# Kernel optimization log

Hardware: AMD Instinct MI355X
Metric: run time of the kernel (lower is better)

The kernel has to match this reference:

```python
import jax, jax.numpy as jnp
import numpy as np

NUM_DAYOFWEEK, NUM_TIME, NUM_MONTH, NUM_DAY = 7, 24, 12, 31
NUM_DESTINATION = 100000
NUM_FACTOR = 128
NUM_DIM = NUM_FACTOR // 4  # 32
N = 1048576


def setup_inputs() -> dict:
    key = jax.random.key(0)
    ks = jax.random.split(key, 10)
    std = 0.1
    return {
        "dayofweek": jax.random.randint(ks[0], (N,), 0, NUM_DAYOFWEEK),
        "time": jax.random.randint(ks[1], (N,), 0, NUM_TIME),
        "month": jax.random.randint(ks[2], (N,), 0, NUM_MONTH),
        "day": jax.random.randint(ks[3], (N,), 0, NUM_DAY),
        "destination": jax.random.randint(ks[4], (N,), 0, NUM_DESTINATION),
        "W_dayofweek": std * jax.random.normal(ks[5], (NUM_DAYOFWEEK, NUM_DIM), dtype=jnp.float32),
        "W_time": std * jax.random.normal(ks[6], (NUM_TIME, NUM_DIM), dtype=jnp.float32),
        "W_month": std * jax.random.normal(ks[7], (NUM_MONTH, NUM_DIM), dtype=jnp.float32),
        "W_day": std * jax.random.normal(ks[8], (NUM_DAY, NUM_DIM), dtype=jnp.float32),
        "W_item": std * jax.random.normal(ks[9], (NUM_DESTINATION, NUM_FACTOR), dtype=jnp.float32),
    }


def reference(dayofweek, time, month, day, destination,
              W_dayofweek, W_time, W_month, W_day, W_item) -> jnp.ndarray:
    # Gather per-feature embeddings and concat into user vector [N, num_factor]
    user = jnp.concatenate([
        W_dayofweek[dayofweek],  # [N, 32]
        W_time[time],            # [N, 32]
        W_month[month],          # [N, 32]
        W_day[day],              # [N, 32]
    ], axis=-1)
    item = W_item[destination]   # [N, 128]
    # Original: diagonal(mm(user, item.T)) == rowwise dot product; compute it directly.
    return jnp.sum(user * item, axis=-1)  # [N]
```

## Files before the change

### kernel.cpp

```cpp
#include <hip/hip_runtime.h>


constexpr int NDIM = 32;
constexpr int SZ_DOW = 7 * NDIM;
constexpr int SZ_TIM = 24 * NDIM;
constexpr int SZ_MON = 12 * NDIM;
constexpr int SZ_DAY = 31 * NDIM;
constexpr int B_DOW = 0;
constexpr int B_TIM = B_DOW + SZ_DOW;
constexpr int B_MON = B_TIM + SZ_TIM;
constexpr int B_DAY = B_MON + SZ_MON;
constexpr int TAB_TOT = B_DAY + SZ_DAY;

__global__ __launch_bounds__(256)
void pack_kernel(const int* __restrict__ dow, const int* __restrict__ tim,
                 const int* __restrict__ mon, const int* __restrict__ day,
                 int* __restrict__ packed, int n) {
    int i = blockIdx.x * blockDim.x + threadIdx.x;
    int stride = gridDim.x * blockDim.x;
    for (; i < n; i += stride)
        packed[i] = dow[i] | (tim[i] << 8) | (mon[i] << 16) | (day[i] << 24);
}

__global__ __launch_bounds__(256, 4)
void mf_mlp_kernel(const int* __restrict__ packed, const int* __restrict__ dest,
                   const float* __restrict__ Wdow, const float* __restrict__ Wtim,
                   const float* __restrict__ Wmon, const float* __restrict__ Wday,
                   const float* __restrict__ Witem,
                   float* __restrict__ out, int n)
{
    __shared__ float tab[TAB_TOT];
    const int tid = threadIdx.x;
    for (int i = tid; i < SZ_DOW; i += 256) tab[B_DOW + i] = Wdow[i];
    for (int i = tid; i < SZ_TIM; i += 256) tab[B_TIM + i] = Wtim[i];
    for (int i = tid; i < SZ_MON; i += 256) tab[B_MON + i] = Wmon[i];
    for (int i = tid; i < SZ_DAY; i += 256) tab[B_DAY + i] = Wday[i];
    __syncthreads();

    const int sub = tid & 63;
    const int wv  = tid >> 6;
    const int g   = sub >> 3;
    const int col = (sub & 7) * 4;
    const int l8  = sub & 7;
    const int tb[4] = {B_DOW, B_TIM, B_MON, B_DAY};

    const long gw     = (long)blockIdx.x * 4 + wv;
    const long nwaves = (long)gridDim.x * 4;

    for (long base = gw * 16; base < n; base += nwaves * 16) {
        const long n0 = base + g;
        const long n1 = base + 8 + g;
        const bool v0 = n0 < n, v1 = n1 < n;

        const int pk0 = v0 ? packed[n0] : 0;
        const int d0  = v0 ? dest[n0]   : 0;
        const int pk1 = v1 ? packed[n1] : 0;
        const int d1  = v1 ? dest[n1]   : 0;

        const float* r0 = Witem + (long)d0 * 128 + col;
        const float* r1 = Witem + (long)d1 * 128 + col;

        float4 it0[4], it1[4], us0[4], us1[4];
#pragma unroll
        for (int j = 0; j < 4; j++) it0[j] = *reinterpret_cast<const float4*>(r0 + j * NDIM);
#pragma unroll
        for (int j = 0; j < 4; j++) it1[j] = *reinterpret_cast<const float4*>(r1 + j * NDIM);
#pragma unroll
        for (int j = 0; j < 4; j++) {
            const int idx = (pk0 >> (8 * j)) & 0xFF;
            us0[j] = *reinterpret_cast<const float4*>(&tab[tb[j] + idx * NDIM + col]);
        }
#pragma unroll
        for (int j = 0; j < 4; j++) {
            const int idx = (pk1 >> (8 * j)) & 0xFF;
            us1[j] = *reinterpret_cast<const float4*>(&tab[tb[j] + idx * NDIM + col]);
        }

        float p0 = 0.f, p1 = 0.f;
#pragma unroll
        for (int j = 0; j < 4; j++) {
            p0 += it0[j].x * us0[j].x + it0[j].y * us0[j].y
                + it0[j].z * us0[j].z + it0[j].w * us0[j].w;
            p1 += it1[j].x * us1[j].x + it1[j].y * us1[j].y
                + it1[j].z * us1[j].z + it1[j].w * us1[j].w;
        }

        p0 += __shfl_xor(p0, 1);  p1 += __shfl_xor(p1, 1);
        p0 += __shfl_xor(p0, 2);  p1 += __shfl_xor(p1, 2);
        p0 += __shfl_xor(p0, 4);  p1 += __shfl_xor(p1, 4);

        if (l8 == 0) {
            if (v0) out[n0] = p0;
            if (v1) out[n1] = p1;
        }
    }
}

__global__ __launch_bounds__(256, 8)
void mf_dot_kernel(const int* __restrict__ dow, const int* __restrict__ tim,
                   const int* __restrict__ mon, const int* __restrict__ day,
                   const int* __restrict__ dest,
                   const float* __restrict__ Wdow, const float* __restrict__ Wtim,
                   const float* __restrict__ Wmon, const float* __restrict__ Wday,
                   const float* __restrict__ Witem,
                   float* __restrict__ out, int n_samples)
{
    __shared__ float tab[TAB_TOT];
    const int tid = threadIdx.x;
    for (int i = tid; i < SZ_DOW; i += 256) tab[B_DOW + i] = Wdow[i];
    for (int i = tid; i < SZ_TIM; i += 256) tab[B_TIM + i] = Wtim[i];
    for (int i = tid; i < SZ_MON; i += 256) tab[B_MON + i] = Wmon[i];
    for (int i = tid; i < SZ_DAY; i += 256) tab[B_DAY + i] = Wday[i];
    __syncthreads();
    const int lane = tid & 63;
    const int sub  = lane & 31;
    const int wave = tid >> 6;
    const int half = lane >> 5;
    const int t    = sub >> 3;
    const int dofs = (sub & 7) * 4;
    const int* idxp  = (t == 0) ? dow   : (t == 1) ? tim   : (t == 2) ? mon   : day;
    const int  tbase = (t == 0) ? B_DOW : (t == 1) ? B_TIM : (t == 2) ? B_MON : B_DAY;
    long n = (long)blockIdx.x * 8 + wave * 2 + half;
    const long stride = (long)gridDim.x * 8;
    for (; n < n_samples; n += stride) {
        const int idx = idxp[n];
        const int ds  = dest[n];
        const float4 u  = *reinterpret_cast<const float4*>(&tab[tbase + idx * NDIM + dofs]);
        const float4 it = *reinterpret_cast<const float4*>(&Witem[(long)ds * 128 + sub * 4]);
        float r = u.x * it.x + u.y * it.y + u.z * it.z + u.w * it.w;
        r += __shfl_xor(r, 16);
        r += __shfl_xor(r, 8);
        r += __shfl_xor(r, 4);
        r += __shfl_xor(r, 2);
        r += __shfl_xor(r, 1);
        if (sub == 0) out[n] = r;
    }
}

extern "C" void kernel_launch(void* const* d_in, const int* in_sizes, int n_in,
                              void* d_out, int out_size, void* d_ws, size_t ws_size,
                              hipStream_t stream)
{
    const int*   dow   = (const int*)d_in[0];
    const int*   tim   = (const int*)d_in[1];
    const int*   mon   = (const int*)d_in[2];
    const int*   day   = (const int*)d_in[3];
    const int*   dest  = (const int*)d_in[4];
    const float* Wdow  = (const float*)d_in[5];
    const float* Wtim  = (const float*)d_in[6];
    const float* Wmon  = (const float*)d_in[7];
    const float* Wday  = (const float*)d_in[8];
    const float* Witem = (const float*)d_in[9];
    float* out = (float*)d_out;

    const int n = in_sizes[0];

    if (ws_size < (size_t)n * sizeof(int)) {
        hipLaunchKernelGGL(mf_dot_kernel, dim3(2048), dim3(256), 0, stream,
                           dow, tim, mon, day, dest,
                           Wdow, Wtim, Wmon, Wday, Witem, out, n);
        return;
    }

    int* packed = (int*)d_ws;
    hipLaunchKernelGGL(pack_kernel, dim3(1024), dim3(256), 0, stream,
                       dow, tim, mon, day, packed, n);
    hipLaunchKernelGGL(mf_mlp_kernel, dim3(2048), dim3(256), 0, stream,
                       packed, dest, Wdow, Wtim, Wmon, Wday, Witem, out, n);
}
```

Measured before the change: 173.8 us.

## Bin samples by destination range for cache-local item table gathers

Replaces the pack+compute pipeline with a counting sort that bins samples into 32 destination ranges (count, scan, scatter of a packed 64-bit payload holding sample index, destination and feature indices). The compute kernel then assigns each block a slice of one bin, with blocks mapped across bins, so concurrent item-row gathers hit a narrow range of W_item that may stay in L2/MALL. The cost is three extra launches, a single-block serial scan, atomics in the scatter, an 8-byte payload written and read per sample, and scattered output writes.

```diff
diff --git a/kernel.cpp b/kernel.cpp
--- a/kernel.cpp
+++ b/kernel.cpp
@@ -2,32 +2,90 @@
 
 
 constexpr int NDIM = 32;
-constexpr int SZ_DOW = 7 * NDIM;
-constexpr int SZ_TIM = 24 * NDIM;
-constexpr int SZ_MON = 12 * NDIM;
-constexpr int SZ_DAY = 31 * NDIM;
+constexpr int SZ_DOW = 7 * NDIM, SZ_TIM = 24 * NDIM, SZ_MON = 12 * NDIM, SZ_DAY = 31 * NDIM;
 constexpr int B_DOW = 0;
 constexpr int B_TIM = B_DOW + SZ_DOW;
 constexpr int B_MON = B_TIM + SZ_TIM;
 constexpr int B_DAY = B_MON + SZ_MON;
 constexpr int TAB_TOT = B_DAY + SZ_DAY;
 
+constexpr int NB   = 32;
+constexpr int DDIV = 3125;
+constexpr int NBLK = 256;
+
 __global__ __launch_bounds__(256)
-void pack_kernel(const int* __restrict__ dow, const int* __restrict__ tim,
-                 const int* __restrict__ mon, const int* __restrict__ day,
-                 int* __restrict__ packed, int n) {
-    int i = blockIdx.x * blockDim.x + threadIdx.x;
-    int stride = gridDim.x * blockDim.x;
-    for (; i < n; i += stride)
-        packed[i] = dow[i] | (tim[i] << 8) | (mon[i] << 16) | (day[i] << 24);
+void count_kernel(const int* __restrict__ dest, int* __restrict__ cnt, int n, int spb) {
+    __shared__ int h[NB];
+    const int t = threadIdx.x, b = blockIdx.x;
+    if (t < NB) h[t] = 0;
+    __syncthreads();
+    const long s0 = (long)b * spb;
+    for (int i = t; i < spb; i += 256) {
+        const long idx = s0 + i;
+        if (idx < n) {
+            int q = dest[idx] / DDIV; if (q > NB - 1) q = NB - 1;
+            atomicAdd(&h[q], 1);
+        }
+    }
+    __syncthreads();
+    if (t < NB) cnt[t * NBLK + b] = h[t];
+}
+
+__global__ __launch_bounds__(256)
+void scan_kernel(int* __restrict__ cntoff, int* __restrict__ bases) {
+    __shared__ int c[NB * NBLK];
+    __shared__ int tot[NB + 1];
+    const int t = threadIdx.x;
+    for (int i = t; i < NB * NBLK; i += 256) c[i] = cntoff[i];
+    __syncthreads();
+    if (t < NB) { int s = 0; for (int b = 0; b < NBLK; b++) s += c[t * NBLK + b]; tot[t] = s; }
+    __syncthreads();
+    if (t == 0) {
+        int run = 0;
+        for (int q = 0; q < NB; q++) { int x = tot[q]; tot[q] = run; run += x; }
+        tot[NB] = run;
+    }
+    __syncthreads();
+    if (t <= NB) bases[t] = tot[t];
+    if (t < NB) {
+        int run = tot[t];
+        for (int b = 0; b < NBLK; b++) { cntoff[t * NBLK + b] = run; run += c[t * NBLK + b]; }
+    }
+}
+
+__global__ __launch_bounds__(256)
+void scatter_kernel(const int* __restrict__ dow, const int* __restrict__ tim,
+                    const int* __restrict__ mon, const int* __restrict__ day,
+                    const int* __restrict__ dest, const int* __restrict__ off,
+                    unsigned long long* __restrict__ payload, int n, int spb) {
+    __shared__ int cur[NB];
+    const int t = threadIdx.x, b = blockIdx.x;
+    if (t < NB) cur[t] = off[t * NBLK + b];
+    __syncthreads();
+    const long s0 = (long)b * spb;
+    for (int i = t; i < spb; i += 256) {
+        const long idx = s0 + i;
+        if (idx < n) {
+            const int ds = dest[idx];
+            int q = ds / DDIV; if (q > NB - 1) q = NB - 1;
+            const int pos = atomicAdd(&cur[q], 1);
+            unsigned long long p = (unsigned long long)(unsigned)idx
+                | ((unsigned long long)(unsigned)ds       << 20)
+                | ((unsigned long long)(unsigned)dow[idx] << 37)
+                | ((unsigned long long)(unsigned)tim[idx] << 40)
+                | ((unsigned long long)(unsigned)mon[idx] << 45)
+                | ((unsigned long long)(unsigned)day[idx] << 49);
+            payload[pos] = p;
+        }
+    }
 }
 
 __global__ __launch_bounds__(256, 4)
-void mf_mlp_kernel(const int* __restrict__ packed, const int* __restrict__ dest,
-                   const float* __restrict__ Wdow, const float* __restrict__ Wtim,
-                   const float* __restrict__ Wmon, const float* __restrict__ Wday,
-                   const float* __restrict__ Witem,
-                   float* __restrict__ out, int n)
+void mf_binned_kernel(const unsigned long long* __restrict__ payload,
+                      const float* __restrict__ Wdow, const float* __restrict__ Wtim,
+                      const float* __restrict__ Wmon, const float* __restrict__ Wday,
+                      const float* __restrict__ Witem,
+                      const int* __restrict__ bases, float* __restrict__ out)
 {
     __shared__ float tab[TAB_TOT];
     const int tid = threadIdx.x;
@@ -40,58 +98,71 @@
     const int sub = tid & 63;
     const int wv  = tid >> 6;
     const int g   = sub >> 3;
-    const int col = (sub & 7) * 4;
     const int l8  = sub & 7;
+    const int col = l8 * 4;
     const int tb[4] = {B_DOW, B_TIM, B_MON, B_DAY};
 
-    const long gw     = (long)blockIdx.x * 4 + wv;
-    const long nwaves = (long)gridDim.x * 4;
-
-    for (long base = gw * 16; base < n; base += nwaves * 16) {
-        const long n0 = base + g;
-        const long n1 = base + 8 + g;
-        const bool v0 = n0 < n, v1 = n1 < n;
-
-        const int pk0 = v0 ? packed[n0] : 0;
-        const int d0  = v0 ? dest[n0]   : 0;
-        const int pk1 = v1 ? packed[n1] : 0;
-        const int d1  = v1 ? dest[n1]   : 0;
-
-        const float* r0 = Witem + (long)d0 * 128 + col;
-        const float* r1 = Witem + (long)d1 * 128 + col;
-
-        float4 it0[4], it1[4], us0[4], us1[4];
-#pragma unroll
-        for (int j = 0; j < 4; j++) it0[j] = *reinterpret_cast<const float4*>(r0 + j * NDIM);
-#pragma unroll
-        for (int j = 0; j < 4; j++) it1[j] = *reinterpret_cast<const float4*>(r1 + j * NDIM);
-#pragma unroll
-        for (int j = 0; j < 4; j++) {
-            const int idx = (pk0 >> (8 * j)) & 0xFF;
-            us0[j] = *reinterpret_cast<const float4*>(&tab[tb[j] + idx * NDIM + col]);
-        }
-#pragma unroll
-        for (int j = 0; j < 4; j++) {
-            const int idx = (pk1 >> (8 * j)) & 0xFF;
-            us1[j] = *reinterpret_cast<const float4*>(&tab[tb[j] + idx * NDIM + col]);
-        }
-
-        float p0 = 0.f, p1 = 0.f;
-#pragma unroll
-        for (int j = 0; j < 4; j++) {
-            p0 += it0[j].x * us0[j].x + it0[j].y * us0[j].y
-                + it0[j].z * us0[j].z + it0[j].w * us0[j].w;
-            p1 += it1[j].x * us1[j].x + it1[j].y * us1[j].y
-                + it1[j].z * us1[j].z + it1[j].w * us1[j].w;
-        }
-
-        p0 += __shfl_xor(p0, 1);  p1 += __shfl_xor(p1, 1);
-        p0 += __shfl_xor(p0, 2);  p1 += __shfl_xor(p1, 2);
-        p0 += __shfl_xor(p0, 4);  p1 += __shfl_xor(p1, 4);
-
-        if (l8 == 0) {
-            if (v0) out[n0] = p0;
-            if (v1) out[n1] = p1;
+    const int x = blockIdx.x & 7;
+    const int s = blockIdx.x >> 3;
+
+    for (int p = 0; p < 4; p++) {
+        const int q  = x + 8 * p;
+        const int qb = bases[q], qe = bases[q + 1];
+        const int len = qe - qb;
+        const int chunk = (len + 255) >> 8;
+        const int st = qb + s * chunk;
+        const int en = min(st + chunk, qe);
+        const int L  = en - st;
+
+        for (int i = wv * 16; i < L; i += 64) {
+            const int i0 = i + g, i1 = i + 8 + g;
+            const bool v0 = i0 < L, v1 = i1 < L;
+
+            const unsigned long long p0 = v0 ? payload[st + i0] : 0ull;
+            const unsigned long long p1 = v1 ? payload[st + i1] : 0ull;
+
+            const int id0 = (int)(p0 & 0xFFFFFull), d0 = (int)((p0 >> 20) & 0x1FFFFull);
+            const int id1 = (int)(p1 & 0xFFFFFull), d1 = (int)((p1 >> 20) & 0x1FFFFull);
+
+            const float* r0 = Witem + (long)d0 * 128 + col;
+            const float* r1 = Witem + (long)d1 * 128 + col;
+
+            float4 it0[4], it1[4], us0[4], us1[4];
+#pragma unroll
+            for (int j = 0; j < 4; j++) it0[j] = *reinterpret_cast<const float4*>(r0 + j * NDIM);
+#pragma unroll
+            for (int j = 0; j < 4; j++) it1[j] = *reinterpret_cast<const float4*>(r1 + j * NDIM);
+
+            const int sh[4] = {37, 40, 45, 49};
+            const int mk[4] = {7, 31, 15, 31};
+#pragma unroll
+            for (int j = 0; j < 4; j++) {
+                const int idx = (int)((p0 >> sh[j]) & (unsigned long long)mk[j]);
+                us0[j] = *reinterpret_cast<const float4*>(&tab[tb[j] + idx * NDIM + col]);
+            }
+#pragma unroll
+            for (int j = 0; j < 4; j++) {
+                const int idx = (int)((p1 >> sh[j]) & (unsigned long long)mk[j]);
+                us1[j] = *reinterpret_cast<const float4*>(&tab[tb[j] + idx * NDIM + col]);
+            }
+
+            float a0 = 0.f, a1 = 0.f;
+#pragma unroll
+            for (int j = 0; j < 4; j++) {
+                a0 += it0[j].x * us0[j].x + it0[j].y * us0[j].y
+                    + it0[j].z * us0[j].z + it0[j].w * us0[j].w;
+                a1 += it1[j].x * us1[j].x + it1[j].y * us1[j].y
+                    + it1[j].z * us1[j].z + it1[j].w * us1[j].w;
+            }
+
+            a0 += __shfl_xor(a0, 1);  a1 += __shfl_xor(a1, 1);
+            a0 += __shfl_xor(a0, 2);  a1 += __shfl_xor(a1, 2);
+            a0 += __shfl_xor(a0, 4);  a1 += __shfl_xor(a1, 4);
+
+            if (l8 == 0) {
+                if (v0) out[id0] = a0;
+                if (v1) out[id1] = a1;
+            }
         }
     }
 }
@@ -112,12 +183,8 @@
     for (int i = tid; i < SZ_MON; i += 256) tab[B_MON + i] = Wmon[i];
     for (int i = tid; i < SZ_DAY; i += 256) tab[B_DAY + i] = Wday[i];
     __syncthreads();
-    const int lane = tid & 63;
-    const int sub  = lane & 31;
-    const int wave = tid >> 6;
-    const int half = lane >> 5;
-    const int t    = sub >> 3;
-    const int dofs = (sub & 7) * 4;
+    const int lane = tid & 63, sub = lane & 31, wave = tid >> 6, half = lane >> 5;
+    const int t = sub >> 3, dofs = (sub & 7) * 4;
     const int* idxp  = (t == 0) ? dow   : (t == 1) ? tim   : (t == 2) ? mon   : day;
     const int  tbase = (t == 0) ? B_DOW : (t == 1) ? B_TIM : (t == 2) ? B_MON : B_DAY;
     long n = (long)blockIdx.x * 8 + wave * 2 + half;
@@ -128,11 +195,8 @@
         const float4 u  = *reinterpret_cast<const float4*>(&tab[tbase + idx * NDIM + dofs]);
         const float4 it = *reinterpret_cast<const float4*>(&Witem[(long)ds * 128 + sub * 4]);
         float r = u.x * it.x + u.y * it.y + u.z * it.z + u.w * it.w;
-        r += __shfl_xor(r, 16);
-        r += __shfl_xor(r, 8);
-        r += __shfl_xor(r, 4);
-        r += __shfl_xor(r, 2);
-        r += __shfl_xor(r, 1);
+        r += __shfl_xor(r, 16); r += __shfl_xor(r, 8); r += __shfl_xor(r, 4);
+        r += __shfl_xor(r, 2);  r += __shfl_xor(r, 1);
         if (sub == 0) out[n] = r;
     }
 }
@@ -155,16 +219,26 @@
 
     const int n = in_sizes[0];
 
-    if (ws_size < (size_t)n * sizeof(int)) {
+    const size_t payload_off = 32 * 1024 + 512;
+    const size_t need = payload_off + (size_t)n * 8;
+
+    if ((size_t)ws_size < need || n > (1 << 20)) {
         hipLaunchKernelGGL(mf_dot_kernel, dim3(2048), dim3(256), 0, stream,
                            dow, tim, mon, day, dest,
                            Wdow, Wtim, Wmon, Wday, Witem, out, n);
         return;
     }
 
-    int* packed = (int*)d_ws;
-    hipLaunchKernelGGL(pack_kernel, dim3(1024), dim3(256), 0, stream,
-                       dow, tim, mon, day, packed, n);
-    hipLaunchKernelGGL(mf_mlp_kernel, dim3(2048), dim3(256), 0, stream,
-                       packed, dest, Wdow, Wtim, Wmon, Wday, Witem, out, n);
-}
+    int* cntoff = (int*)d_ws;
+    int* bases  = (int*)((char*)d_ws + 32 * 1024);
+    unsigned long long* payload = (unsigned long long*)((char*)d_ws + payload_off);
+
+    const int spb = (n + NBLK - 1) / NBLK;
+
+    hipLaunchKernelGGL(count_kernel,   dim3(NBLK), dim3(256), 0, stream, dest, cntoff, n, spb);
+    hipLaunchKernelGGL(scan_kernel,    dim3(1),    dim3(256), 0, stream, cntoff, bases);
+    hipLaunchKernelGGL(scatter_kernel, dim3(NBLK), dim3(256), 0, stream,
+                       dow, tim, mon, day, dest, cntoff, payload, n, spb);
+    hipLaunchKernelGGL(mf_binned_kernel, dim3(2048), dim3(256), 0, stream,
+                       payload, Wdow, Wtim, Wmon, Wday, Witem, bases, out);
+}
```

After: 183.6 us. 1.06x slower.
